# Kernel tuning notes

Measured on AMD Instinct MI355X. Metric: run time of the kernel, lower is better.

Reference implementation:

```python
import jax, jax.numpy as jnp
import numpy as np
from jax import lax

B, C_IN, H = 64, 3, 64
K_FEAT, KSIZE, STRIDE = 24, 8, 8
G_IN, G_HID, F_HID, OUT = 52, 256, 256, 1


def setup_inputs() -> dict:
    key = jax.random.key(0)
    ks = jax.random.split(key, 8)
    s = lambda fan_in: 1.0 / np.sqrt(fan_in)
    return {
        "image": jax.random.normal(ks[0], (B, C_IN, H, H), jnp.float32),
        "conv_w": jax.random.normal(ks[1], (K_FEAT, C_IN, KSIZE, KSIZE), jnp.float32) * s(C_IN * KSIZE * KSIZE),
        "conv_b": jnp.zeros((K_FEAT,), jnp.float32),
        "g_w1": jax.random.normal(ks[2], (G_IN, G_HID), jnp.float32) * s(G_IN),
        "g_b1": jnp.zeros((G_HID,), jnp.float32),
        "g_w2": jax.random.normal(ks[3], (G_HID, G_HID), jnp.float32) * s(G_HID),
        "g_b2": jnp.zeros((G_HID,), jnp.float32),
        "f_w1": jax.random.normal(ks[4], (G_HID, F_HID), jnp.float32) * s(G_HID),
        "f_b1": jnp.zeros((F_HID,), jnp.float32),
        "f_w2": jax.random.normal(ks[5], (F_HID, OUT), jnp.float32) * s(F_HID),
        "f_b2": jnp.zeros((OUT,), jnp.float32),
    }


def reference(image, conv_w, conv_b, g_w1, g_b1, g_w2, g_b2, f_w1, f_b1, f_w2, f_b2):
    # feature_extractor: conv k8/s8 + ReLU -> (B, k, d, d)
    x = lax.conv_general_dilated(image, conv_w, (STRIDE, STRIDE), "VALID",
                                 dimension_numbers=("NCHW", "OIHW", "NCHW"))
    x = jax.nn.relu(x + conv_b[None, :, None, None])
    b, k, d, _ = x.shape
    # coordinate channels: x varies along columns, y along rows (linspace(-1,1,d))
    coord = jnp.linspace(-1.0, 1.0, d, dtype=x.dtype)
    cx = jnp.broadcast_to(coord[None, None, None, :], (b, 1, d, d))
    cy = jnp.broadcast_to(coord[None, None, :, None], (b, 1, d, d))
    x = jnp.concatenate([x, cx, cy], axis=1)          # (B, k+2, d, d)
    k2 = k + 2
    x = x.reshape(b, k2, d * d).transpose(0, 2, 1)     # (B, d^2, k+2)
    # all-pairs: pair (i, j) -> concat(x[:, j], x[:, i])  (matches repeat/cat in torch)
    left = jnp.broadcast_to(x[:, None, :, :], (b, d * d, d * d, k2))
    right = jnp.broadcast_to(x[:, :, None, :], (b, d * d, d * d, k2))
    pairs = jnp.concatenate([left, right], axis=-1)    # (B, d^2, d^2, 2(k+2))
    # g: shared MLP over pairs
    h = jax.nn.relu(pairs @ g_w1 + g_b1)
    h = jax.nn.relu(h @ g_w2 + g_b2)                   # (B, d^2, d^2, 256)
    pooled = jnp.sum(h, axis=(1, 2))                   # sum over d^4 pairs -> (B, 256)
    # f: head MLP
    h = jax.nn.relu(pooled @ f_w1 + f_b1)
    return h @ f_w2 + f_b2                             # (B, 1)
```

## Files before the change

### kernel.cpp

```cpp
#include <hip/hip_runtime.h>
#include <hip/hip_bf16.h>
#include <stdint.h>


typedef float f32x4 __attribute__((ext_vector_type(4)));
typedef float f32x2 __attribute__((ext_vector_type(2)));
typedef short short8 __attribute__((ext_vector_type(8)));
typedef int   int4v  __attribute__((ext_vector_type(4)));

#define NB 4

__device__ __forceinline__ uint32_t cvt_pk_bf16(float lo, float hi) {
    uint32_t r;
    asm("v_cvt_pk_bf16_f32 %0, %1, %2" : "=v"(r) : "v"(lo), "v"(hi));
    return r;
}
__device__ __forceinline__ f32x2 relu2(f32x2 a) {
    f32x2 z = (f32x2){0.f, 0.f};
    return __builtin_elementwise_max(a, z);
}
__device__ __forceinline__ uint32_t fuse2(uint32_t up, float vlo, float vhi) {
    f32x2 uu;
    uu.x = __uint_as_float(up << 16);
    uu.y = __uint_as_float(up & 0xFFFF0000u);
    f32x2 r = relu2(uu + (f32x2){vlo, vhi});
    return cvt_pk_bf16(r.x, r.y);
}
__device__ __forceinline__ void spin_eq(int* p, int val) {
    while (__hip_atomic_load(p, __ATOMIC_ACQUIRE, __HIP_MEMORY_SCOPE_WORKGROUP) != val)
        __builtin_amdgcn_s_sleep(1);
    __builtin_amdgcn_sched_barrier(0);
}
__device__ __forceinline__ void flag_release_add(int* p, int lane) {
    asm volatile("s_waitcnt lgkmcnt(0)" ::: "memory");
    if (lane == 0)
        __hip_atomic_fetch_add(p, 1, __ATOMIC_RELEASE, __HIP_MEMORY_SCOPE_WORKGROUP);
}

__global__ void k12_front(const float* __restrict__ img, const float* __restrict__ cw,
                          const float* __restrict__ cb, const float* __restrict__ w1,
                          const float* __restrict__ b1, const float* __restrict__ w2,
                          float* __restrict__ u, float* __restrict__ v,
                          short* __restrict__ w2f) {
    int g = blockIdx.x;
    int t = threadIdx.x;
    if (g >= 256) {
        int fi = (g - 256) * 4 + (t >> 6);
        int l = t & 63;
        int ks = fi >> 4, ni2 = fi & 15;
        int n  = ni2 * 16 + (l & 15);
        int k0 = ks * 32 + (l >> 4) * 8;
        float f[8];
        #pragma unroll
        for (int e = 0; e < 8; ++e) f[e] = w2[(k0 + e) * 256 + n];
        union { short8 s; uint32_t w[4]; } A;
        A.w[0] = cvt_pk_bf16(f[0], f[1]);
        A.w[1] = cvt_pk_bf16(f[2], f[3]);
        A.w[2] = cvt_pk_bf16(f[4], f[5]);
        A.w[3] = cvt_pk_bf16(f[6], f[7]);
        *(short8*)(w2f + (fi * 64 + l) * 8) = A.s;
        return;
    }
    __shared__ float xs[16][26];
    int b = g >> 2, q = g & 3, p0 = q * 16;

    for (int idx = t; idx < 416; idx += 256) {
        int pl = idx / 26;
        int ch = idx - pl * 26;
        int pos = p0 + pl;
        int r = pos >> 3, c = pos & 7;
        float val;
        if (ch < 24) {
            float s = cb[ch];
            #pragma unroll
            for (int ci = 0; ci < 3; ++ci)
                #pragma unroll
                for (int kr = 0; kr < 8; ++kr) {
                    const float* ip = img + ((b * 3 + ci) * 64 + r * 8 + kr) * 64 + c * 8;
                    const float* wp = cw + ((ch * 3 + ci) * 8 + kr) * 8;
                    #pragma unroll
                    for (int kc = 0; kc < 8; ++kc) s += ip[kc] * wp[kc];
                }
            val = fmaxf(s, 0.f);
        } else if (ch == 24) {
            val = -1.f + (2.f / 7.f) * (float)c;
        } else {
            val = -1.f + (2.f / 7.f) * (float)r;
        }
        xs[pl][ch] = val;
    }
    __syncthreads();

    int c = t;
    float bc = b1[c];
    float su[16], sv[16];
    #pragma unroll
    for (int r = 0; r < 16; ++r) { su[r] = bc; sv[r] = 0.f; }
    #pragma unroll 2
    for (int k = 0; k < 26; ++k) {
        float wu = w1[k * 256 + c];
        float wv2 = w1[(26 + k) * 256 + c];
        #pragma unroll
        for (int r = 0; r < 16; ++r) {
            float xv = xs[r][k];
            su[r] += xv * wu;
            sv[r] += xv * wv2;
        }
    }
    #pragma unroll
    for (int r = 0; r < 16; ++r) {
        int bj = b * 64 + p0 + r;
        u[bj * 256 + c] = su[r];
        v[bj * 256 + c] = sv[r];
    }
}

#define C_READ(A, KS)                                                  \
    { A[0] = *(const short8*)(cb0 + (KS) * 1024);                      \
      A[1] = *(const short8*)(cb0 + 8192  + (KS) * 1024);              \
      A[2] = *(const short8*)(cb0 + 16384 + (KS) * 1024);              \
      A[3] = *(const short8*)(cb0 + 24576 + (KS) * 1024); }

#define C_MFMA(A, KS)                                                  \
    { acc[0][0] = __builtin_amdgcn_mfma_f32_16x16x32_bf16(A[0], Bf[KS][0], acc[0][0], 0,0,0); \
      acc[1][0] = __builtin_amdgcn_mfma_f32_16x16x32_bf16(A[1], Bf[KS][0], acc[1][0], 0,0,0); \
      acc[2][0] = __builtin_amdgcn_mfma_f32_16x16x32_bf16(A[2], Bf[KS][0], acc[2][0], 0,0,0); \
      acc[3][0] = __builtin_amdgcn_mfma_f32_16x16x32_bf16(A[3], Bf[KS][0], acc[3][0], 0,0,0); \
      acc[0][1] = __builtin_amdgcn_mfma_f32_16x16x32_bf16(A[0], Bf[KS][1], acc[0][1], 0,0,0); \
      acc[1][1] = __builtin_amdgcn_mfma_f32_16x16x32_bf16(A[1], Bf[KS][1], acc[1][1], 0,0,0); \
      acc[2][1] = __builtin_amdgcn_mfma_f32_16x16x32_bf16(A[2], Bf[KS][1], acc[2][1], 0,0,0); \
      acc[3][1] = __builtin_amdgcn_mfma_f32_16x16x32_bf16(A[3], Bf[KS][1], acc[3][1], 0,0,0); }

__global__ __launch_bounds__(768, 3) void k3_pairs(
        const float* __restrict__ u, const float* __restrict__ v,
        const short* __restrict__ w2f, const float* __restrict__ b2,
        float* __restrict__ part) {
    __shared__ short h1s[NB][64 * 256];
    __shared__ float vs[16][256];
    __shared__ int prod_cnt[16];
    __shared__ int cons_cnt[16];
    int t = threadIdx.x;
    int lane = t & 63, wv = t >> 6;
    int lr = lane & 15, lg = lane >> 4;
    int blk = blockIdx.x;
    int b = blk & 63, i0 = (blk >> 6) * 16;

    if (t < 16) { prod_cnt[t] = 0; cons_cnt[t] = 0; }

    if (t < 512) {
        int q = t >> 5, c8 = (t & 31) * 8;
        const float* vr = v + (b * 64 + i0 + q) * 256 + c8;
        *(float4*)&vs[q][c8]     = *(const float4*)vr;
        *(float4*)&vs[q][c8 + 4] = *(const float4*)(vr + 4);
    }

    if (wv < 4) {
        uint32_t upk[8][4];
        #pragma unroll
        for (int j = 0; j < 8; ++j) {
            int fid = j * 4 + wv;
            int row = (fid >> 3) * 16 + lr;
            int k0 = (fid & 7) * 32 + lg * 8;
            const float* up = u + (b * 64 + row) * 256 + k0;
            f32x4 x0 = *(const f32x4*)up;
            f32x4 x1 = *(const f32x4*)(up + 4);
            upk[j][0] = cvt_pk_bf16(x0.x, x0.y);
            upk[j][1] = cvt_pk_bf16(x0.z, x0.w);
            upk[j][2] = cvt_pk_bf16(x1.x, x1.y);
            upk[j][3] = cvt_pk_bf16(x1.z, x1.w);
        }
        __syncthreads();

        #pragma unroll 1
        for (int q = 0; q < 16; ++q) {
            if (q >= NB) spin_eq(&cons_cnt[q - NB], 8);
            char* base = (char*)h1s[q & (NB - 1)] + lane * 16;
            #pragma unroll
            for (int j = 0; j < 8; ++j) {
                int fid = j * 4 + wv;
                int k0 = (fid & 7) * 32 + lg * 8;
                f32x4 v0 = *(const f32x4*)&vs[q][k0];
                f32x4 v1 = *(const f32x4*)&vs[q][k0 + 4];
                int4v d;
                d.x = (int)fuse2(upk[j][0], v0.x, v0.y);
                d.y = (int)fuse2(upk[j][1], v0.z, v0.w);
                d.z = (int)fuse2(upk[j][2], v1.x, v1.y);
                d.w = (int)fuse2(upk[j][3], v1.z, v1.w);
                *(int4v*)(base + fid * 1024) = d;
            }
            flag_release_add(&prod_cnt[q], lane);
        }
    } else {
        int wc = wv - 4;

        short8 Bf[8][2];
        #pragma unroll
        for (int ks = 0; ks < 8; ++ks)
            #pragma unroll
            for (int cg = 0; cg < 2; ++cg)
                Bf[ks][cg] = *(const short8*)(w2f + ((ks * 16 + wc * 2 + cg) * 64 + lane) * 8);

        float bias[2];
        #pragma unroll
        for (int cg = 0; cg < 2; ++cg) bias[cg] = b2[wc * 32 + cg * 16 + lr];

        float csum[2] = {0.f, 0.f};
        __syncthreads();

        #pragma unroll 1
        for (int q = 0; q < 16; ++q) {
            spin_eq(&prod_cnt[q], 4);
            const char* cb0 = (const char*)h1s[q & (NB - 1)] + lane * 16;

            f32x4 acc[4][2];
            #pragma unroll
            for (int mi = 0; mi < 4; ++mi)
                #pragma unroll
                for (int cg = 0; cg < 2; ++cg) acc[mi][cg] = (f32x4){0.f, 0.f, 0.f, 0.f};

            short8 Aa[4], Ab[4];
            C_READ(Aa, 0) C_READ(Ab, 1)
            __builtin_amdgcn_s_setprio(1);
            C_MFMA(Aa, 0) C_READ(Aa, 2)
            C_MFMA(Ab, 1) C_READ(Ab, 3)
            C_MFMA(Aa, 2) C_READ(Aa, 4)
            C_MFMA(Ab, 3) C_READ(Ab, 5)
            C_MFMA(Aa, 4) C_READ(Aa, 6)
            C_MFMA(Ab, 5) C_READ(Ab, 7)
            C_MFMA(Aa, 6)
            C_MFMA(Ab, 7)
            __builtin_amdgcn_s_setprio(0);

            #pragma unroll
            for (int cg = 0; cg < 2; ++cg) {
                float s = 0.f;
                #pragma unroll
                for (int mi = 0; mi < 4; ++mi)
                    #pragma unroll
                    for (int r = 0; r < 4; ++r)
                        s += fmaxf(acc[mi][cg][r] + bias[cg], 0.f);
                csum[cg] += s;
            }
            flag_release_add(&cons_cnt[q], lane);
        }

        #pragma unroll
        for (int cg = 0; cg < 2; ++cg) {
            float s = csum[cg];
            s += __shfl_xor(s, 16);
            s += __shfl_xor(s, 32);
            if (lane < 16) part[(blk * 8 + wc) * 32 + cg * 16 + lr] = s;
        }
    }
}

__global__ void k5_head(const float* __restrict__ part, const float* __restrict__ fw1,
                        const float* __restrict__ fb1, const float* __restrict__ fw2,
                        const float* __restrict__ fb2, float* __restrict__ out) {
    __shared__ float P[256];
    __shared__ float wsum[4];
    int b = blockIdx.x, t = threadIdx.x;
    int wc = t >> 5, cl = t & 31;
    float s0 = 0.f;
    #pragma unroll
    for (int g = 0; g < 4; ++g)
        s0 += part[((b + 64 * g) * 8 + wc) * 32 + cl];
    P[t] = s0;
    __syncthreads();
    float a0 = 0.f, a1 = 0.f, a2 = 0.f, a3 = 0.f;
    for (int k = 0; k < 64; ++k) {
        a0 += P[k]       * fw1[k * 256 + t];
        a1 += P[k + 64]  * fw1[(k + 64) * 256 + t];
        a2 += P[k + 128] * fw1[(k + 128) * 256 + t];
        a3 += P[k + 192] * fw1[(k + 192) * 256 + t];
    }
    float h = fmaxf(fb1[t] + a0 + a1 + a2 + a3, 0.f);
    float p = h * fw2[t];
    #pragma unroll
    for (int off = 32; off >= 1; off >>= 1) p += __shfl_xor(p, off);
    if ((t & 63) == 0) wsum[t >> 6] = p;
    __syncthreads();
    if (t == 0) out[b] = wsum[0] + wsum[1] + wsum[2] + wsum[3] + fb2[0];
}

extern "C" void kernel_launch(void* const* d_in, const int* in_sizes, int n_in,
                              void* d_out, int out_size, void* d_ws, size_t ws_size,
                              hipStream_t stream) {
    const float* image  = (const float*)d_in[0];
    const float* conv_w = (const float*)d_in[1];
    const float* conv_b = (const float*)d_in[2];
    const float* g_w1   = (const float*)d_in[3];
    const float* g_b1   = (const float*)d_in[4];
    const float* g_w2   = (const float*)d_in[5];
    const float* g_b2   = (const float*)d_in[6];
    const float* f_w1   = (const float*)d_in[7];
    const float* f_b1   = (const float*)d_in[8];
    const float* f_w2   = (const float*)d_in[9];
    const float* f_b2   = (const float*)d_in[10];
    float* out = (float*)d_out;

    char* ws = (char*)d_ws;
    float* u    = (float*)(ws + 0);
    float* v    = (float*)(ws + 4194304);
    short* w2f  = (short*)(ws + 8388608);
    float* part = (float*)(ws + 8519680);

    k12_front<<<288, 256, 0, stream>>>(image, conv_w, conv_b, g_w1, g_b1, g_w2,
                                       u, v, w2f);
    k3_pairs<<<256, 768, 0, stream>>>(u, v, w2f, g_b2, part);
    k5_head<<<64, 256, 0, stream>>>(part, f_w1, f_b1, f_w2, f_b2, out);
}
```

Before: 60.25 us.

## Switch pair GEMM from 16x16x32 to 32x32x16 MFMA with matching layouts

Replaces the 16x16x32 bf16 MFMA tiling in the consumer waves with 32x32x16 MFMAs. The W2 fragment layout, the producer's h1 fragment layout and the u loads are all remapped to the 32x32 operand format. Two independent accumulator chains per M-tile (even and odd K steps) are summed before the bias and ReLU reduction. Each LDS A-read now feeds a larger MFMA, cutting LDS read traffic and instruction count per FLOP, at the cost of 16-wide accumulators (more VGPRs) and longer MFMA latency chains.

Measured after the change: 62.20 us. +3.2%, slower.

```diff
diff --git a/kernel.cpp b/kernel.cpp
--- a/kernel.cpp
+++ b/kernel.cpp
@@ -3,8 +3,9 @@
 #include <stdint.h>
 
 
-typedef float f32x4 __attribute__((ext_vector_type(4)));
-typedef float f32x2 __attribute__((ext_vector_type(2)));
+typedef float f32x4  __attribute__((ext_vector_type(4)));
+typedef float f32x2  __attribute__((ext_vector_type(2)));
+typedef float f32x16 __attribute__((ext_vector_type(16)));
 typedef short short8 __attribute__((ext_vector_type(8)));
 typedef int   int4v  __attribute__((ext_vector_type(4)));
 
@@ -47,9 +48,9 @@
     if (g >= 256) {
         int fi = (g - 256) * 4 + (t >> 6);
         int l = t & 63;
-        int ks = fi >> 4, ni2 = fi & 15;
-        int n  = ni2 * 16 + (l & 15);
-        int k0 = ks * 32 + (l >> 4) * 8;
+        int ks = fi >> 3, nt = fi & 7;
+        int n  = nt * 32 + (l & 31);
+        int k0 = ks * 16 + (l >> 5) * 8;
         float f[8];
         #pragma unroll
         for (int e = 0; e < 8; ++e) f[e] = w2[(k0 + e) * 256 + n];
@@ -115,21 +116,13 @@
     }
 }
 
-#define C_READ(A, KS)                                                  \
+#define RD(A, KS)                                                      \
     { A[0] = *(const short8*)(cb0 + (KS) * 1024);                      \
-      A[1] = *(const short8*)(cb0 + 8192  + (KS) * 1024);              \
-      A[2] = *(const short8*)(cb0 + 16384 + (KS) * 1024);              \
-      A[3] = *(const short8*)(cb0 + 24576 + (KS) * 1024); }
-
-#define C_MFMA(A, KS)                                                  \
-    { acc[0][0] = __builtin_amdgcn_mfma_f32_16x16x32_bf16(A[0], Bf[KS][0], acc[0][0], 0,0,0); \
-      acc[1][0] = __builtin_amdgcn_mfma_f32_16x16x32_bf16(A[1], Bf[KS][0], acc[1][0], 0,0,0); \
-      acc[2][0] = __builtin_amdgcn_mfma_f32_16x16x32_bf16(A[2], Bf[KS][0], acc[2][0], 0,0,0); \
-      acc[3][0] = __builtin_amdgcn_mfma_f32_16x16x32_bf16(A[3], Bf[KS][0], acc[3][0], 0,0,0); \
-      acc[0][1] = __builtin_amdgcn_mfma_f32_16x16x32_bf16(A[0], Bf[KS][1], acc[0][1], 0,0,0); \
-      acc[1][1] = __builtin_amdgcn_mfma_f32_16x16x32_bf16(A[1], Bf[KS][1], acc[1][1], 0,0,0); \
-      acc[2][1] = __builtin_amdgcn_mfma_f32_16x16x32_bf16(A[2], Bf[KS][1], acc[2][1], 0,0,0); \
-      acc[3][1] = __builtin_amdgcn_mfma_f32_16x16x32_bf16(A[3], Bf[KS][1], acc[3][1], 0,0,0); }
+      A[1] = *(const short8*)(cb0 + (16 + (KS)) * 1024); }
+
+#define MM(A, KS, P)                                                   \
+    acc[0][P] = __builtin_amdgcn_mfma_f32_32x32x16_bf16(A[0], Bf[KS], acc[0][P], 0, 0, 0); \
+    acc[1][P] = __builtin_amdgcn_mfma_f32_32x32x16_bf16(A[1], Bf[KS], acc[1][P], 0, 0, 0);
 
 __global__ __launch_bounds__(768, 3) void k3_pairs(
         const float* __restrict__ u, const float* __restrict__ v,
@@ -141,7 +134,6 @@
     __shared__ int cons_cnt[16];
     int t = threadIdx.x;
     int lane = t & 63, wv = t >> 6;
-    int lr = lane & 15, lg = lane >> 4;
     int blk = blockIdx.x;
     int b = blk & 63, i0 = (blk >> 6) * 16;
 
@@ -159,8 +151,8 @@
         #pragma unroll
         for (int j = 0; j < 8; ++j) {
             int fid = j * 4 + wv;
-            int row = (fid >> 3) * 16 + lr;
-            int k0 = (fid & 7) * 32 + lg * 8;
+            int row = (fid >> 4) * 32 + (lane & 31);
+            int k0 = (fid & 15) * 16 + (lane >> 5) * 8;
             const float* up = u + (b * 64 + row) * 256 + k0;
             f32x4 x0 = *(const f32x4*)up;
             f32x4 x1 = *(const f32x4*)(up + 4);
@@ -178,7 +170,7 @@
             #pragma unroll
             for (int j = 0; j < 8; ++j) {
                 int fid = j * 4 + wv;
-                int k0 = (fid & 7) * 32 + lg * 8;
+                int k0 = (fid & 15) * 16 + (lane >> 5) * 8;
                 f32x4 v0 = *(const f32x4*)&vs[q][k0];
                 f32x4 v1 = *(const f32x4*)&vs[q][k0 + 4];
                 int4v d;
@@ -193,18 +185,13 @@
     } else {
         int wc = wv - 4;
 
-        short8 Bf[8][2];
+        short8 Bf[16];
         #pragma unroll
-        for (int ks = 0; ks < 8; ++ks)
-            #pragma unroll
-            for (int cg = 0; cg < 2; ++cg)
-                Bf[ks][cg] = *(const short8*)(w2f + ((ks * 16 + wc * 2 + cg) * 64 + lane) * 8);
-
-        float bias[2];
-        #pragma unroll
-        for (int cg = 0; cg < 2; ++cg) bias[cg] = b2[wc * 32 + cg * 16 + lr];
-
-        float csum[2] = {0.f, 0.f};
+        for (int ks = 0; ks < 16; ++ks)
+            Bf[ks] = *(const short8*)(w2f + ((ks * 8 + wc) * 64 + lane) * 8);
+
+        float bias = b2[wc * 32 + (lane & 31)];
+        float csum = 0.f;
         __syncthreads();
 
         #pragma unroll 1
@@ -212,45 +199,49 @@
             spin_eq(&prod_cnt[q], 4);
             const char* cb0 = (const char*)h1s[q & (NB - 1)] + lane * 16;
 
-            f32x4 acc[4][2];
+            f32x16 acc[2][2];
             #pragma unroll
-            for (int mi = 0; mi < 4; ++mi)
+            for (int mi = 0; mi < 2; ++mi)
                 #pragma unroll
-                for (int cg = 0; cg < 2; ++cg) acc[mi][cg] = (f32x4){0.f, 0.f, 0.f, 0.f};
-
-            short8 Aa[4], Ab[4];
-            C_READ(Aa, 0) C_READ(Ab, 1)
+                for (int p = 0; p < 2; ++p)
+                    #pragma unroll
+                    for (int r = 0; r < 16; ++r) acc[mi][p][r] = 0.f;
+
+            short8 Aa[2], Ab[2];
+            RD(Aa, 0) RD(Ab, 1)
             __builtin_amdgcn_s_setprio(1);
-            C_MFMA(Aa, 0) C_READ(Aa, 2)
-            C_MFMA(Ab, 1) C_READ(Ab, 3)
-            C_MFMA(Aa, 2) C_READ(Aa, 4)
-            C_MFMA(Ab, 3) C_READ(Ab, 5)
-            C_MFMA(Aa, 4) C_READ(Aa, 6)
-            C_MFMA(Ab, 5) C_READ(Ab, 7)
-            C_MFMA(Aa, 6)
-            C_MFMA(Ab, 7)
+            MM(Aa, 0, 0)  RD(Aa, 2)
+            MM(Ab, 1, 1)  RD(Ab, 3)
+            MM(Aa, 2, 0)  RD(Aa, 4)
+            MM(Ab, 3, 1)  RD(Ab, 5)
+            MM(Aa, 4, 0)  RD(Aa, 6)
+            MM(Ab, 5, 1)  RD(Ab, 7)
+            MM(Aa, 6, 0)  RD(Aa, 8)
+            MM(Ab, 7, 1)  RD(Ab, 9)
+            MM(Aa, 8, 0)  RD(Aa, 10)
+            MM(Ab, 9, 1)  RD(Ab, 11)
+            MM(Aa, 10, 0) RD(Aa, 12)
+            MM(Ab, 11, 1) RD(Ab, 13)
+            MM(Aa, 12, 0) RD(Aa, 14)
+            MM(Ab, 13, 1) RD(Ab, 15)
+            MM(Aa, 14, 0)
+            MM(Ab, 15, 1)
             __builtin_amdgcn_s_setprio(0);
 
             #pragma unroll
-            for (int cg = 0; cg < 2; ++cg) {
+            for (int mi = 0; mi < 2; ++mi) {
+                f32x16 cfull = acc[mi][0] + acc[mi][1];
                 float s = 0.f;
                 #pragma unroll
-                for (int mi = 0; mi < 4; ++mi)
-                    #pragma unroll
-                    for (int r = 0; r < 4; ++r)
-                        s += fmaxf(acc[mi][cg][r] + bias[cg], 0.f);
-                csum[cg] += s;
+                for (int r = 0; r < 16; ++r)
+                    s += fmaxf(cfull[r] + bias, 0.f);
+                csum += s;
             }
             flag_release_add(&cons_cnt[q], lane);
         }
 
-        #pragma unroll
-        for (int cg = 0; cg < 2; ++cg) {
-            float s = csum[cg];
-            s += __shfl_xor(s, 16);
-            s += __shfl_xor(s, 32);
-            if (lane < 16) part[(blk * 8 + wc) * 32 + cg * 16 + lr] = s;
-        }
+        csum += __shfl_xor(csum, 32);
+        if (lane < 32) part[(blk * 8 + wc) * 32 + (lane & 31)] = csum;
     }
 }
 
```
